# Kernel optimization log

Hardware: AMD Instinct MI355X
Metric: run time of the kernel (lower is better)

Reference implementation:

```python
import jax, jax.numpy as jnp
import numpy as np

B = 128
D = 256


def _offsets(lengths):
    # complete (exclusive->inclusive) cumsum with leading zero, like fbgemm asynchronous_complete_cumsum
    return jnp.concatenate([jnp.zeros((1,), lengths.dtype), jnp.cumsum(lengths)])


def jagged_concat2(v0, l0, v1, l1):
    # Per-sample concat of two jagged 2D tensors (same batch size B).
    # v0: [sum(l0), D], v1: [sum(l1), D]. Output: [sum(l0)+sum(l1), D].
    out_len = l0 + l1
    off_out = _offsets(out_len)
    off0 = _offsets(l0)
    off1 = _offsets(l1)
    total = v0.shape[0] + v1.shape[0]  # static
    p = jnp.arange(total, dtype=l0.dtype)
    s = jnp.searchsorted(off_out, p, side='right') - 1  # sample id per output row
    pos = p - off_out[s]                                # position within sample
    from0 = pos < l0[s]
    idx0 = jnp.clip(off0[s] + pos, 0, v0.shape[0] - 1)
    idx1 = jnp.clip(off1[s] + pos - l0[s], 0, v1.shape[0] - 1)
    out = jnp.where(from0[:, None], v0[idx0], v1[idx1])
    return out, out_len


def setup_inputs() -> dict:
    key = jax.random.key(0)
    k1, k2, k3, k4 = jax.random.split(key, 4)
    # ragged item lengths alternating 512/1536 -> sum = B*1024 = 131072
    item_lengths = np.where(np.arange(B) % 2 == 0, 512, 1536).astype(np.int32)
    n_items = int(item_lengths.sum())
    return {
        'item_values': jax.random.normal(k1, (n_items, D), dtype=jnp.float32),
        'action_values': jax.random.normal(k2, (n_items, D), dtype=jnp.float32),
        'ctx0_values': jax.random.normal(k3, (B, D), dtype=jnp.float32),
        'ctx1_values': jax.random.normal(k4, (B, D), dtype=jnp.float32),
        'item_lengths': jnp.asarray(item_lengths),
        'ctx0_lengths': jnp.ones((B,), dtype=jnp.int32),
        'ctx1_lengths': jnp.ones((B,), dtype=jnp.int32),
    }


def reference(item_values, action_values, ctx0_values, ctx1_values,
              item_lengths, ctx0_lengths, ctx1_lengths):
    # 1) Interleave item/action per token: cat(dim=1).view(2N, D)
    n = item_values.shape[0]
    seq = jnp.stack([item_values, action_values], axis=1).reshape(2 * n, D)
    seq_len = item_lengths * 2
    # 2) Per-sample concat of contextual features (jagged_2D_tensor_concat)
    ctx_vals, ctx_len = jagged_concat2(ctx0_values, ctx0_lengths, ctx1_values, ctx1_lengths)
    # 3) Per-sample concat [contextual, interleaved sequence]
    out_vals, out_len = jagged_concat2(ctx_vals, ctx_len, seq, seq_len)
    return out_vals, out_len.astype(jnp.int32)
```

## Files before the change

kernel.cpp:

```cpp
#include <hip/hip_runtime.h>

#define D 256
#define MAXB 128

typedef float f32x4 __attribute__((ext_vector_type(4)));

__global__ __launch_bounds__(256) void hstu_preproc_fused(
    const float* __restrict__ item, const float* __restrict__ action,
    const float* __restrict__ c0v, const float* __restrict__ c1v,
    const int* __restrict__ item_len, const int* __restrict__ c0_len,
    const int* __restrict__ c1_len,
    float* __restrict__ out, int total_rows, int Bn) {
    __shared__ int s_oo[MAXB + 1];
    __shared__ int s_io[MAXB + 1];
    __shared__ int s_c0[MAXB + 1];
    __shared__ int s_c1[MAXB + 1];

    int t = threadIdx.x;
    int li = 0, l0 = 0, l1 = 0;
    if (t < Bn) {
        li = item_len[t];
        l0 = c0_len[t];
        l1 = c1_len[t];
    }
    if (t == 0) { s_oo[0] = 0; s_io[0] = 0; s_c0[0] = 0; s_c1[0] = 0; }
    if (t < Bn) {
        s_oo[t + 1] = 2 * li + l0 + l1;
        s_io[t + 1] = li;
        s_c0[t + 1] = l0;
        s_c1[t + 1] = l1;
    }
    __syncthreads();
    for (int off = 1; off < Bn; off <<= 1) {
        int a = 0, b = 0, c = 0, d = 0;
        int idx = t + 1;
        bool act = (t < Bn) && (idx > off);
        if (act) {
            a = s_oo[idx - off];
            b = s_io[idx - off];
            c = s_c0[idx - off];
            d = s_c1[idx - off];
        }
        __syncthreads();
        if (act) {
            s_oo[idx] += a;
            s_io[idx] += b;
            s_c0[idx] += c;
            s_c1[idx] += d;
        }
        __syncthreads();
    }

    if (blockIdx.x == 0 && t < Bn) {
        out[(size_t)total_rows * D + t] = (float)(s_oo[t + 1] - s_oo[t]);
    }

    int wave = t >> 6;
    int lane = t & 63;
    int gwave = blockIdx.x * 4 + wave;
    int nwaves = gridDim.x * 4;

    for (int r = gwave; r < total_rows; r += nwaves) {
        int lo = 0, hi = Bn;
        while (hi - lo > 1) {
            int mid = (lo + hi) >> 1;
            if (r >= s_oo[mid]) lo = mid; else hi = mid;
        }
        int s = lo;
        int pos = r - s_oo[s];
        int l0c = s_c0[s + 1] - s_c0[s];
        int l1c = s_c1[s + 1] - s_c1[s];

        const float* src;
        if (pos < l0c) {
            src = c0v + (size_t)(s_c0[s] + pos) * D;
        } else if (pos < l0c + l1c) {
            src = c1v + (size_t)(s_c1[s] + pos - l0c) * D;
        } else {
            int q = pos - l0c - l1c;
            int tk = s_io[s] + (q >> 1);
            src = ((q & 1) ? action : item) + (size_t)tk * D;
        }

        f32x4 v = __builtin_nontemporal_load(
            reinterpret_cast<const f32x4*>(src) + lane);
        __builtin_nontemporal_store(
            v, reinterpret_cast<f32x4*>(out + (size_t)r * D) + lane);
    }
}

extern "C" void kernel_launch(void* const* d_in, const int* in_sizes, int n_in,
                              void* d_out, int out_size, void* d_ws, size_t ws_size,
                              hipStream_t stream) {
    const float* item   = (const float*)d_in[0];
    const float* action = (const float*)d_in[1];
    const float* c0v    = (const float*)d_in[2];
    const float* c1v    = (const float*)d_in[3];
    const int* item_len = (const int*)d_in[4];
    const int* c0_len   = (const int*)d_in[5];
    const int* c1_len   = (const int*)d_in[6];
    float* out = (float*)d_out;

    int Bn = in_sizes[4];
    int total_rows = (out_size - Bn) / D;

    int grid = 2048;
    hstu_preproc_fused<<<grid, 256, 0, stream>>>(
        item, action, c0v, c1v, item_len, c0_len, c1_len, out, total_rows, Bn);
}
```

Before: 96.04 us.

## Split row copy into context pass and per-token item/action pair pass

Reworks the gather loop from one output row per wave iteration into two loops. One loop copies the contextual rows, indexed over context rows. The other handles one token per iteration, loading the item and action rows together and storing both interleaved output rows. This halves the binary searches and loop iterations for the dominant sequence part and gives each wave two independent loads in flight, at the cost of two separate loop phases.

```diff
diff --git a/kernel.cpp b/kernel.cpp
--- a/kernel.cpp
+++ b/kernel.cpp
@@ -10,7 +10,7 @@
     const float* __restrict__ c0v, const float* __restrict__ c1v,
     const int* __restrict__ item_len, const int* __restrict__ c0_len,
     const int* __restrict__ c1_len,
-    float* __restrict__ out, int total_rows, int Bn) {
+    float* __restrict__ out, int total_rows, int total_tok, int Bn) {
     __shared__ int s_oo[MAXB + 1];
     __shared__ int s_io[MAXB + 1];
     __shared__ int s_c0[MAXB + 1];
@@ -60,32 +60,45 @@
     int gwave = blockIdx.x * 4 + wave;
     int nwaves = gridDim.x * 4;
 
-    for (int r = gwave; r < total_rows; r += nwaves) {
+    int totc = s_c0[Bn] + s_c1[Bn];
+    for (int c = gwave; c < totc; c += nwaves) {
         int lo = 0, hi = Bn;
         while (hi - lo > 1) {
             int mid = (lo + hi) >> 1;
-            if (r >= s_oo[mid]) lo = mid; else hi = mid;
+            if (c >= s_c0[mid] + s_c1[mid]) lo = mid; else hi = mid;
         }
         int s = lo;
-        int pos = r - s_oo[s];
+        int pos = c - (s_c0[s] + s_c1[s]);
         int l0c = s_c0[s + 1] - s_c0[s];
-        int l1c = s_c1[s + 1] - s_c1[s];
-
-        const float* src;
-        if (pos < l0c) {
-            src = c0v + (size_t)(s_c0[s] + pos) * D;
-        } else if (pos < l0c + l1c) {
-            src = c1v + (size_t)(s_c1[s] + pos - l0c) * D;
-        } else {
-            int q = pos - l0c - l1c;
-            int tk = s_io[s] + (q >> 1);
-            src = ((q & 1) ? action : item) + (size_t)tk * D;
-        }
-
+        const float* src = (pos < l0c)
+            ? c0v + (size_t)(s_c0[s] + pos) * D
+            : c1v + (size_t)(s_c1[s] + pos - l0c) * D;
+        int orow = s_oo[s] + pos;
         f32x4 v = __builtin_nontemporal_load(
             reinterpret_cast<const f32x4*>(src) + lane);
         __builtin_nontemporal_store(
-            v, reinterpret_cast<f32x4*>(out + (size_t)r * D) + lane);
+            v, reinterpret_cast<f32x4*>(out + (size_t)orow * D) + lane);
+    }
+
+    for (int tk = gwave; tk < total_tok; tk += nwaves) {
+        int lo = 0, hi = Bn;
+        while (hi - lo > 1) {
+            int mid = (lo + hi) >> 1;
+            if (tk >= s_io[mid]) lo = mid; else hi = mid;
+        }
+        int s = lo;
+        int l0c = s_c0[s + 1] - s_c0[s];
+        int l1c = s_c1[s + 1] - s_c1[s];
+        int orow = s_oo[s] + l0c + l1c + 2 * (tk - s_io[s]);
+
+        f32x4 vi = __builtin_nontemporal_load(
+            reinterpret_cast<const f32x4*>(item + (size_t)tk * D) + lane);
+        f32x4 va = __builtin_nontemporal_load(
+            reinterpret_cast<const f32x4*>(action + (size_t)tk * D) + lane);
+
+        float* dst = out + (size_t)orow * D;
+        __builtin_nontemporal_store(vi, reinterpret_cast<f32x4*>(dst) + lane);
+        __builtin_nontemporal_store(va, reinterpret_cast<f32x4*>(dst + D) + lane);
     }
 }
 
@@ -103,8 +116,10 @@
 
     int Bn = in_sizes[4];
     int total_rows = (out_size - Bn) / D;
+    int total_tok  = in_sizes[0] / D;
 
     int grid = 2048;
     hstu_preproc_fused<<<grid, 256, 0, stream>>>(
-        item, action, c0v, c1v, item_len, c0_len, c1_len, out, total_rows, Bn);
+        item, action, c0v, c1v, item_len, c0_len, c1_len,
+        out, total_rows, total_tok, Bn);
 }
```

Measured after the change: 98.91 us. 3.0% more time.
